# Kernel tuning notes

Hardware: AMD Instinct MI355X
Metric: run time of the kernel (lower is better)

Reference implementation:

```python
import jax, jax.numpy as jnp
from jax import lax
import numpy as np

DATA_DIM, DATA_NUM, CTX_DIM, PB_DIM, HID_DIM, T = 6, 30, 180, 2, 240, 8192


def setup_inputs() -> dict:
    key = jax.random.key(0)
    ks = jax.random.split(key, 12)
    f = lambda k, s: jax.random.normal(k, s, dtype=jnp.float32)
    return {
        "data": f(ks[0], (DATA_NUM, DATA_DIM, T)),
        "W1d": f(ks[1], (HID_DIM, DATA_DIM)) * 0.1,
        "b1d": f(ks[2], (HID_DIM,)) * 0.1,
        "W1p": f(ks[3], (HID_DIM, PB_DIM)) * 0.1,
        "b1p": f(ks[4], (HID_DIM,)) * 0.1,
        "W1c": f(ks[5], (HID_DIM, CTX_DIM)) * 0.05,
        "b1c": f(ks[6], (HID_DIM,)) * 0.1,
        "W2d": f(ks[7], (DATA_DIM, HID_DIM)) * 0.1,
        "b2d": f(ks[8], (DATA_DIM,)) * 0.1,
        "W2c": f(ks[9], (CTX_DIM, HID_DIM)) * 0.05,
        "b2c": f(ks[10], (CTX_DIM,)) * 0.1,
        "pb": f(ks[11], (DATA_NUM, PB_DIM)) * 0.1,
    }


def reference(data, W1d, b1d, W1p, b1p, W1c, b1c, W2d, b2d, W2c, b2c, pb):
    # Teacher-forcing path (GENERATE=False): each timestep's input is data[:, :, t];
    # only ctx is carried through the recurrence.
    # Precompute the time-varying + pb input projections for all steps: [T, B, H]
    pre = (jnp.einsum('bdt,hd->tbh', data, W1d) + b1d
           + (pb @ W1p.T + b1p)[None, :, :])

    def step(ctx, pre_t):
        h = jax.nn.relu(pre_t + ctx @ W1c.T + b1c)   # [B, H]
        out = h @ W2d.T + b2d                        # [B, data_dim]
        new_ctx = h @ W2c.T + b2c                    # [B, ctx_dim]
        return new_ctx, out

    ctx0 = jnp.zeros((data.shape[0], CTX_DIM), dtype=data.dtype)
    _, outs = lax.scan(step, ctx0, pre)              # outs: [T, B, data_dim]
    return jnp.transpose(outs, (1, 0, 2))            # [B, T, data_dim] (stack dim=1)
```

## Files before the change

### kernel.cpp

```cpp
#include <hip/hip_runtime.h>
#include <hip/hip_bf16.h>
#include <stdint.h>


#define T_STEPS 8192
#define HID     240
#define CTX     180
#define KTOT    256
#define HXBUF   4096
#define A_HALVES (256*256)
#define SCRATCH_BYTES (A_HALVES*2 + 16)

typedef __hip_bfloat16 bf16;
typedef _Float16 f16;
typedef _Float16 half8  __attribute__((ext_vector_type(8)));
typedef _Float16 half4v __attribute__((ext_vector_type(4)));
typedef float    f32x4  __attribute__((ext_vector_type(4)));
typedef float    f32x2  __attribute__((ext_vector_type(2)));

#define MFMA16(A,B,C) __builtin_amdgcn_mfma_f32_16x16x32_f16((A),(B),(C),0,0,0)

__device__ __forceinline__ float ldin(const void* p, long i, bool f32) {
    return f32 ? ((const float*)p)[i] : __bfloat162float(((const bf16*)p)[i]);
}
__device__ __forceinline__ unsigned pkbf(float a, float b) {
    unsigned ua = (unsigned)__builtin_bit_cast(unsigned short, __float2bfloat16(a));
    unsigned ub = (unsigned)__builtin_bit_cast(unsigned short, __float2bfloat16(b));
    return ua | (ub << 16);
}
__device__ __forceinline__ void barrier_lds() {
    asm volatile("s_waitcnt lgkmcnt(0)\n\ts_barrier" ::: "memory");
}

__global__ __launch_bounds__(64) void detect_dtype(const void* data, int* flag) {
    unsigned int w  = ((const unsigned int*)data)[threadIdx.x];
    unsigned int lo = w & 0xFFFFu;
    unsigned int ex = (lo >> 7) & 0xFFu;
    unsigned long long huge = __ballot(ex >= 0x8Eu);
    unsigned long long zero = __ballot(lo == 0u);
    if (threadIdx.x == 0) *flag = (huge != 0ull || zero == ~0ull) ? 1 : 0;
}

__global__ __launch_bounds__(256) void build_A(
    const void* __restrict__ W1d, const void* __restrict__ b1d,
    const void* __restrict__ W1p, const void* __restrict__ b1p,
    const void* __restrict__ W1c, const void* __restrict__ b1c,
    const void* __restrict__ W2d, const void* __restrict__ b2d,
    const void* __restrict__ W2c, const void* __restrict__ b2c,
    f16* __restrict__ Aa, const int* __restrict__ flagp)
{
    const bool f32 = (*flagp != 0);
    int idx = blockIdx.x*256 + threadIdx.x;
    int r = idx >> 8, k = idx & 255;
    float v = 0.f;
    if (r < HID) {
        if (k < HID) {
            float acc = 0.f;
            for (int c = 0; c < CTX; ++c)
                acc = fmaf(ldin(W1c, r*CTX+c, f32), ldin(W2c, c*HID+k, f32), acc);
            v = acc;
        } else if (k < 246) {
            v = ldin(W1d, r*6 + (k-240), f32);
        } else if (k == 246) {
            float m0 = 0.f;
            for (int c = 0; c < CTX; ++c)
                m0 = fmaf(ldin(W1c, r*CTX+c, f32), ldin(b2c, c, f32), m0);
            v = ldin(b1d, r, f32) + ldin(b1c, r, f32) + ldin(b1p, r, f32) + m0;
        } else if (k <= 248) {
            v = ldin(W1p, r*2 + (k-247), f32);
        }
    } else if (r < 246) {
        int o = r - 240;
        if (k < HID)       v = ldin(W2d, o*HID + k, f32);
        else if (k == 246) v = ldin(b2d, o, f32);
    }
    Aa[idx] = (f16)v;
}

__device__ __forceinline__ int hx_off(int j, int n) {
    return (j >> 5)*512 + ((((j & 31) >> 3))*16 + n)*8 + (j & 7);
}

__global__ __launch_bounds__(512, 2) void rnn_mfma(
    const void* __restrict__ data,
    const void* __restrict__ b1d, const void* __restrict__ W1p,
    const void* __restrict__ b1p, const void* __restrict__ b1c,
    const void* __restrict__ W1d, const void* __restrict__ pb,
    const f16* __restrict__ Aa, const int* __restrict__ flagp,
    void* __restrict__ out)
{
    const bool f32 = (*flagp != 0);
    const int tid  = threadIdx.x;
    const int w    = tid >> 6;
    const int l    = tid & 63;
    const int n16  = l & 15;
    const int quad = l >> 4;
    const int base = blockIdx.x * 16;
    const int bn   = base + n16;
    const bool bvalid = (bn < 30);

    __shared__ __align__(16) f16 Hx[2*HXBUF];

    {
        int* hz = (int*)Hx;
        for (int i = tid; i < HXBUF; i += 512) hz[i] = 0;
    }
    __syncthreads();

    if (tid < 32) {
        int bsel = tid >> 4, n = tid & 15;
        int nb = base + n; if (nb > 29) nb = 29;
        f16* buf = Hx + bsel*HXBUF;
        buf[3584 + (32+n)*8 + 6] = (f16)1.0f;
        buf[3584 + (32+n)*8 + 7] = (f16)ldin(pb, nb*2+0, f32);
        buf[3584 + (48+n)*8 + 0] = (f16)ldin(pb, nb*2+1, f32);
    }

    for (int p = tid; p < HID*16; p += 512) {
        int n = p / HID, j = p - n*HID;
        int nb = base + n; if (nb > 29) nb = 29;
        float s = ldin(b1d, j, f32) + ldin(b1c, j, f32) + ldin(b1p, j, f32)
                + ldin(W1p, j*2+0, f32)*ldin(pb, nb*2+0, f32)
                + ldin(W1p, j*2+1, f32)*ldin(pb, nb*2+1, f32);
        for (int d = 0; d < 6; ++d)
            s = fmaf(ldin(W1d, j*6+d, f32), ldin(data, ((long)nb*6+d)*T_STEPS, f32), s);
        Hx[hx_off(j, n)] = (f16)fmaxf(s, 0.f);
    }

    const int pn = tid & 15, pd = tid >> 4;
    int pnb = base + pn; if (pnb > 29) pnb = 29;
    const long prow = ((long)pnb*6 + (pd < 6 ? pd : 0))*T_STEPS;
    const int  doff = 3584 + (32+pn)*8 + pd;

    if (tid < 96)
        Hx[doff] = (f16)ldin(data, prow + 1, f32);

    unsigned u0 = 0, u1 = 0;
    if (tid < 96) {
        if (!f32) {
            u0 = ((const unsigned short*)data)[prow + 2];
            u1 = ((const unsigned short*)data)[prow + 3];
        } else {
            u0 = __builtin_bit_cast(unsigned, ((const float*)data)[prow + 2]);
            u1 = __builtin_bit_cast(unsigned, ((const float*)data)[prow + 3]);
        }
    }

    const f16* Ab0 = Aa + (size_t)((w*2+0)*16 + n16)*KTOT + quad*8;
    const f16* Ab1 = Aa + (size_t)((w*2+1)*16 + n16)*KTOT + quad*8;
    half8 a00 = *(const half8*)(Ab0 +   0), a01 = *(const half8*)(Ab0 +  32);
    half8 a02 = *(const half8*)(Ab0 +  64), a03 = *(const half8*)(Ab0 +  96);
    half8 a04 = *(const half8*)(Ab0 + 128), a05 = *(const half8*)(Ab0 + 160);
    half8 a06 = *(const half8*)(Ab0 + 192), a07 = *(const half8*)(Ab0 + 224);
    half8 a10 = *(const half8*)(Ab1 +   0), a11 = *(const half8*)(Ab1 +  32);
    half8 a12 = *(const half8*)(Ab1 +  64), a13 = *(const half8*)(Ab1 +  96);
    half8 a14 = *(const half8*)(Ab1 + 128), a15 = *(const half8*)(Ab1 + 160);
    half8 a16 = *(const half8*)(Ab1 + 192), a17 = *(const half8*)(Ab1 + 224);
    asm volatile("s_waitcnt vmcnt(0)" ::: "memory");
    __syncthreads();

    const f16* hxread0 = Hx + l*8;
    f16* hxw = Hx + w*512 + ((quad>>1)*16 + n16)*8 + 4*(quad&1);

    for (int t2 = 0; t2 < T_STEPS; t2 += 2) {
        #pragma unroll
        for (int s = 0; s < 2; ++s) {
            const int t = t2 + s;
            const int cur = s, nxt = s ^ 1;

            if (tid < 96) {
                unsigned uc = (s == 0) ? u0 : u1;
                float dv = f32 ? __builtin_bit_cast(float, uc)
                               : __builtin_bit_cast(float, uc << 16);
                Hx[nxt*HXBUF + doff] = (f16)dv;
                long g = t + 4; if (g > T_STEPS-1) g = T_STEPS-1;
                unsigned un;
                if (!f32) un = ((const unsigned short*)data)[prow + g];
                else      un = __builtin_bit_cast(unsigned, ((const float*)data)[prow + g]);
                if (s == 0) u0 = un; else u1 = un;
            }

            const f16* hxc = hxread0 + cur*HXBUF;
            half8 b0 = *(const half8*)(hxc +    0);
            half8 b1 = *(const half8*)(hxc +  512);
            half8 b2 = *(const half8*)(hxc + 1024);
            f32x4 c0 = {0.f,0.f,0.f,0.f}, c1 = {0.f,0.f,0.f,0.f};
            half8 b3 = *(const half8*)(hxc + 1536);
            c0 = MFMA16(a00, b0, c0);  c1 = MFMA16(a10, b0, c1);
            half8 b4 = *(const half8*)(hxc + 2048);
            c0 = MFMA16(a01, b1, c0);  c1 = MFMA16(a11, b1, c1);
            half8 b5 = *(const half8*)(hxc + 2560);
            c0 = MFMA16(a02, b2, c0);  c1 = MFMA16(a12, b2, c1);
            half8 b6 = *(const half8*)(hxc + 3072);
            c0 = MFMA16(a03, b3, c0);  c1 = MFMA16(a13, b3, c1);
            half8 b7 = *(const half8*)(hxc + 3584);
            c0 = MFMA16(a04, b4, c0);  c1 = MFMA16(a14, b4, c1);
            c0 = MFMA16(a05, b5, c0);  c1 = MFMA16(a15, b5, c1);
            c0 = MFMA16(a06, b6, c0);  c1 = MFMA16(a16, b6, c1);
            c0 = MFMA16(a07, b7, c0);  c1 = MFMA16(a17, b7, c1);

            f16* hxn = hxw + nxt*HXBUF;
            {
                half4v hv;
                hv.x = (f16)fmaxf(c0.x, 0.f);
                hv.y = (f16)fmaxf(c0.y, 0.f);
                hv.z = (f16)fmaxf(c0.z, 0.f);
                hv.w = (f16)fmaxf(c0.w, 0.f);
                *(half4v*)(hxn) = hv;
            }
            if (w < 7) {
                half4v hv;
                hv.x = (f16)fmaxf(c1.x, 0.f);
                hv.y = (f16)fmaxf(c1.y, 0.f);
                hv.z = (f16)fmaxf(c1.z, 0.f);
                hv.w = (f16)fmaxf(c1.w, 0.f);
                *(half4v*)(hxn + 256) = hv;
            } else if (bvalid) {
                long ob = ((long)bn*T_STEPS + t)*6;
                if (quad == 0) {
                    if (!f32) {
                        bf16* op = (bf16*)out + ob;
                        *(unsigned*)(op)     = pkbf(c1.x, c1.y);
                        *(unsigned*)(op + 2) = pkbf(c1.z, c1.w);
                    } else {
                        float* op = (float*)out + ob;
                        f32x2 p0 = {c1.x, c1.y}; *(f32x2*)(op)     = p0;
                        f32x2 p1 = {c1.z, c1.w}; *(f32x2*)(op + 2) = p1;
                    }
                } else if (quad == 1) {
                    if (!f32) {
                        bf16* op = (bf16*)out + ob;
                        *(unsigned*)(op + 4) = pkbf(c1.x, c1.y);
                    } else {
                        float* op = (float*)out + ob;
                        f32x2 p0 = {c1.x, c1.y}; *(f32x2*)(op + 4) = p0;
                    }
                }
            }
            barrier_lds();
        }
    }
}

extern "C" void kernel_launch(void* const* d_in, const int* in_sizes, int n_in,
                              void* d_out, int out_size, void* d_ws, size_t ws_size,
                              hipStream_t stream) {
    const void* data = d_in[0];
    const void* W1d  = d_in[1];
    const void* b1d  = d_in[2];
    const void* W1p  = d_in[3];
    const void* b1p  = d_in[4];
    const void* W1c  = d_in[5];
    const void* b1c  = d_in[6];
    const void* W2d  = d_in[7];
    const void* b2d  = d_in[8];
    const void* W2c  = d_in[9];
    const void* b2c  = d_in[10];
    const void* pb   = d_in[11];

    size_t need = SCRATCH_BYTES;
    char* scratch;
    if (ws_size >= need) {
        scratch = (char*)d_ws;
    } else {
        size_t out_bytes = (size_t)30*T_STEPS*6*sizeof(bf16);
        scratch = (char*)d_out + ((out_bytes - need) & ~(size_t)255);
    }
    f16* Aa    = (f16*)scratch;
    int* flagp = (int*)(scratch + A_HALVES*2);

    detect_dtype<<<1, 64, 0, stream>>>(data, flagp);
    build_A<<<A_HALVES/256, 256, 0, stream>>>(W1d, b1d, W1p, b1p, W1c, b1c,
                                              W2d, b2d, W2c, b2c, Aa, flagp);
    rnn_mfma<<<2, 512, 0, stream>>>(data, b1d, W1p, b1p, b1c, W1d, pb,
                                    Aa, flagp, d_out);
}
```

Baseline: 3.977 ms.

## Split K dimension across wave pairs with LDS partial-sum exchange

```diff
diff --git a/kernel.cpp b/kernel.cpp
--- a/kernel.cpp
+++ b/kernel.cpp
@@ -8,6 +8,7 @@
 #define CTX     180
 #define KTOT    256
 #define HXBUF   4096
+#define PBUF    4096
 #define A_HALVES (256*256)
 #define SCRATCH_BYTES (A_HALVES*2 + 16)
 
@@ -92,6 +93,9 @@
     const bool f32 = (*flagp != 0);
     const int tid  = threadIdx.x;
     const int w    = tid >> 6;
+    const int P    = w & 3;
+    const int role = w >> 2;
+    const int vw   = P*2 + role;
     const int l    = tid & 63;
     const int n16  = l & 15;
     const int quad = l >> 4;
@@ -99,7 +103,7 @@
     const int bn   = base + n16;
     const bool bvalid = (bn < 30);
 
-    __shared__ __align__(16) f16 Hx[2*HXBUF];
+    __shared__ __align__(16) f16 Hx[2*HXBUF + PBUF];
 
     {
         int* hz = (int*)Hx;
@@ -146,21 +150,22 @@
         }
     }
 
-    const f16* Ab0 = Aa + (size_t)((w*2+0)*16 + n16)*KTOT + quad*8;
-    const f16* Ab1 = Aa + (size_t)((w*2+1)*16 + n16)*KTOT + quad*8;
-    half8 a00 = *(const half8*)(Ab0 +   0), a01 = *(const half8*)(Ab0 +  32);
-    half8 a02 = *(const half8*)(Ab0 +  64), a03 = *(const half8*)(Ab0 +  96);
-    half8 a04 = *(const half8*)(Ab0 + 128), a05 = *(const half8*)(Ab0 + 160);
-    half8 a06 = *(const half8*)(Ab0 + 192), a07 = *(const half8*)(Ab0 + 224);
-    half8 a10 = *(const half8*)(Ab1 +   0), a11 = *(const half8*)(Ab1 +  32);
-    half8 a12 = *(const half8*)(Ab1 +  64), a13 = *(const half8*)(Ab1 +  96);
-    half8 a14 = *(const half8*)(Ab1 + 128), a15 = *(const half8*)(Ab1 + 160);
-    half8 a16 = *(const half8*)(Ab1 + 192), a17 = *(const half8*)(Ab1 + 224);
+    const f16* Ab = Aa + (size_t)((4*P)*16 + n16)*KTOT + role*128 + quad*8;
+    half8 A00 = *(const half8*)(Ab +     0 +  0), A01 = *(const half8*)(Ab +     0 + 32);
+    half8 A02 = *(const half8*)(Ab +     0 + 64), A03 = *(const half8*)(Ab +     0 + 96);
+    half8 A10 = *(const half8*)(Ab +  4096 +  0), A11 = *(const half8*)(Ab +  4096 + 32);
+    half8 A12 = *(const half8*)(Ab +  4096 + 64), A13 = *(const half8*)(Ab +  4096 + 96);
+    half8 A20 = *(const half8*)(Ab +  8192 +  0), A21 = *(const half8*)(Ab +  8192 + 32);
+    half8 A22 = *(const half8*)(Ab +  8192 + 64), A23 = *(const half8*)(Ab +  8192 + 96);
+    half8 A30 = *(const half8*)(Ab + 12288 +  0), A31 = *(const half8*)(Ab + 12288 + 32);
+    half8 A32 = *(const half8*)(Ab + 12288 + 64), A33 = *(const half8*)(Ab + 12288 + 96);
     asm volatile("s_waitcnt vmcnt(0)" ::: "memory");
     __syncthreads();
 
-    const f16* hxread0 = Hx + l*8;
-    f16* hxw = Hx + w*512 + ((quad>>1)*16 + n16)*8 + 4*(quad&1);
+    const f16* hxread0 = Hx + role*2048 + l*8;
+    f16* hxw = Hx + vw*512 + ((quad>>1)*16 + n16)*8 + 4*(quad&1);
+    f16*       pwr = Hx + 2*HXBUF + (P*2 + role)*512     + l*4;
+    const f16* prd = Hx + 2*HXBUF + (P*2 + (role^1))*512 + l*4;
 
     for (int t2 = 0; t2 < T_STEPS; t2 += 2) {
         #pragma unroll
@@ -183,57 +188,74 @@
             const f16* hxc = hxread0 + cur*HXBUF;
             half8 b0 = *(const half8*)(hxc +    0);
             half8 b1 = *(const half8*)(hxc +  512);
+            f32x4 c0 = {0.f,0.f,0.f,0.f}, c1 = {0.f,0.f,0.f,0.f};
+            f32x4 c2 = {0.f,0.f,0.f,0.f}, c3 = {0.f,0.f,0.f,0.f};
             half8 b2 = *(const half8*)(hxc + 1024);
-            f32x4 c0 = {0.f,0.f,0.f,0.f}, c1 = {0.f,0.f,0.f,0.f};
+            c0 = MFMA16(A00, b0, c0);  c1 = MFMA16(A10, b0, c1);
+            c2 = MFMA16(A20, b0, c2);  c3 = MFMA16(A30, b0, c3);
             half8 b3 = *(const half8*)(hxc + 1536);
-            c0 = MFMA16(a00, b0, c0);  c1 = MFMA16(a10, b0, c1);
-            half8 b4 = *(const half8*)(hxc + 2048);
-            c0 = MFMA16(a01, b1, c0);  c1 = MFMA16(a11, b1, c1);
-            half8 b5 = *(const half8*)(hxc + 2560);
-            c0 = MFMA16(a02, b2, c0);  c1 = MFMA16(a12, b2, c1);
-            half8 b6 = *(const half8*)(hxc + 3072);
-            c0 = MFMA16(a03, b3, c0);  c1 = MFMA16(a13, b3, c1);
-            half8 b7 = *(const half8*)(hxc + 3584);
-            c0 = MFMA16(a04, b4, c0);  c1 = MFMA16(a14, b4, c1);
-            c0 = MFMA16(a05, b5, c0);  c1 = MFMA16(a15, b5, c1);
-            c0 = MFMA16(a06, b6, c0);  c1 = MFMA16(a16, b6, c1);
-            c0 = MFMA16(a07, b7, c0);  c1 = MFMA16(a17, b7, c1);
+            c0 = MFMA16(A01, b1, c0);  c1 = MFMA16(A11, b1, c1);
+            c2 = MFMA16(A21, b1, c2);  c3 = MFMA16(A31, b1, c3);
+            c0 = MFMA16(A02, b2, c0);  c1 = MFMA16(A12, b2, c1);
+            c2 = MFMA16(A22, b2, c2);  c3 = MFMA16(A32, b2, c3);
+            c0 = MFMA16(A03, b3, c0);  c1 = MFMA16(A13, b3, c1);
+            c2 = MFMA16(A23, b3, c2);  c3 = MFMA16(A33, b3, c3);
+
+            if (role == 0) {
+                half4v w0; w0.x=(f16)c2.x; w0.y=(f16)c2.y; w0.z=(f16)c2.z; w0.w=(f16)c2.w;
+                half4v w1; w1.x=(f16)c3.x; w1.y=(f16)c3.y; w1.z=(f16)c3.z; w1.w=(f16)c3.w;
+                *(half4v*)(pwr)       = w0;
+                *(half4v*)(pwr + 256) = w1;
+            } else {
+                half4v w0; w0.x=(f16)c0.x; w0.y=(f16)c0.y; w0.z=(f16)c0.z; w0.w=(f16)c0.w;
+                half4v w1; w1.x=(f16)c1.x; w1.y=(f16)c1.y; w1.z=(f16)c1.z; w1.w=(f16)c1.w;
+                *(half4v*)(pwr)       = w0;
+                *(half4v*)(pwr + 256) = w1;
+            }
+            barrier_lds();
+
+            half4v p0 = *(const half4v*)(prd);
+            half4v p1 = *(const half4v*)(prd + 256);
+            f32x4 o0 = (role == 0) ? c0 : c2;
+            f32x4 o1 = (role == 0) ? c1 : c3;
 
             f16* hxn = hxw + nxt*HXBUF;
             {
                 half4v hv;
-                hv.x = (f16)fmaxf(c0.x, 0.f);
-                hv.y = (f16)fmaxf(c0.y, 0.f);
-                hv.z = (f16)fmaxf(c0.z, 0.f);
-                hv.w = (f16)fmaxf(c0.w, 0.f);
+                hv.x = (f16)fmaxf(o0.x + (float)p0.x, 0.f);
+                hv.y = (f16)fmaxf(o0.y + (float)p0.y, 0.f);
+                hv.z = (f16)fmaxf(o0.z + (float)p0.z, 0.f);
+                hv.w = (f16)fmaxf(o0.w + (float)p0.w, 0.f);
                 *(half4v*)(hxn) = hv;
             }
-            if (w < 7) {
+            if (vw < 7) {
                 half4v hv;
-                hv.x = (f16)fmaxf(c1.x, 0.f);
-                hv.y = (f16)fmaxf(c1.y, 0.f);
-                hv.z = (f16)fmaxf(c1.z, 0.f);
-                hv.w = (f16)fmaxf(c1.w, 0.f);
+                hv.x = (f16)fmaxf(o1.x + (float)p1.x, 0.f);
+                hv.y = (f16)fmaxf(o1.y + (float)p1.y, 0.f);
+                hv.z = (f16)fmaxf(o1.z + (float)p1.z, 0.f);
+                hv.w = (f16)fmaxf(o1.w + (float)p1.w, 0.f);
                 *(half4v*)(hxn + 256) = hv;
             } else if (bvalid) {
+                float v0 = o1.x + (float)p1.x, v1 = o1.y + (float)p1.y;
+                float v2 = o1.z + (float)p1.z, v3 = o1.w + (float)p1.w;
                 long ob = ((long)bn*T_STEPS + t)*6;
                 if (quad == 0) {
                     if (!f32) {
                         bf16* op = (bf16*)out + ob;
-                        *(unsigned*)(op)     = pkbf(c1.x, c1.y);
-                        *(unsigned*)(op + 2) = pkbf(c1.z, c1.w);
+                        *(unsigned*)(op)     = pkbf(v0, v1);
+                        *(unsigned*)(op + 2) = pkbf(v2, v3);
                     } else {
                         float* op = (float*)out + ob;
-                        f32x2 p0 = {c1.x, c1.y}; *(f32x2*)(op)     = p0;
-                        f32x2 p1 = {c1.z, c1.w}; *(f32x2*)(op + 2) = p1;
+                        f32x2 q0 = {v0, v1}; *(f32x2*)(op)     = q0;
+                        f32x2 q1 = {v2, v3}; *(f32x2*)(op + 2) = q1;
                     }
                 } else if (quad == 1) {
                     if (!f32) {
                         bf16* op = (bf16*)out + ob;
-                        *(unsigned*)(op + 4) = pkbf(c1.x, c1.y);
+                        *(unsigned*)(op + 4) = pkbf(v0, v1);
                     } else {
                         float* op = (float*)out + ob;
-                        f32x2 p0 = {c1.x, c1.y}; *(f32x2*)(op + 4) = p0;
+                        f32x2 q0 = {v0, v1}; *(f32x2*)(op + 4) = q0;
                     }
                 }
             }
```

Result: slower. 5.643 ms (+41.9%).

## Defer output stores a step, interleave MFMA chains, hoist LDS loads

Applied to the files above, without the earlier changes.

```diff
diff --git a/kernel.cpp b/kernel.cpp
--- a/kernel.cpp
+++ b/kernel.cpp
@@ -30,6 +30,28 @@
 }
 __device__ __forceinline__ void barrier_lds() {
     asm volatile("s_waitcnt lgkmcnt(0)\n\ts_barrier" ::: "memory");
+}
+
+__device__ __forceinline__ void store_out(void* out, bool f32, int quad, long ob, f32x4 v) {
+    if (quad == 0) {
+        if (!f32) {
+            bf16* op = (bf16*)out + ob;
+            *(unsigned*)(op)     = pkbf(v.x, v.y);
+            *(unsigned*)(op + 2) = pkbf(v.z, v.w);
+        } else {
+            float* op = (float*)out + ob;
+            f32x2 p0 = {v.x, v.y}; *(f32x2*)(op)     = p0;
+            f32x2 p1 = {v.z, v.w}; *(f32x2*)(op + 2) = p1;
+        }
+    } else if (quad == 1) {
+        if (!f32) {
+            bf16* op = (bf16*)out + ob;
+            *(unsigned*)(op + 4) = pkbf(v.x, v.y);
+        } else {
+            float* op = (float*)out + ob;
+            f32x2 p0 = {v.x, v.y}; *(f32x2*)(op + 4) = p0;
+        }
+    }
 }
 
 __global__ __launch_bounds__(64) void detect_dtype(const void* data, int* flag) {
@@ -98,6 +120,7 @@
     const int base = blockIdx.x * 16;
     const int bn   = base + n16;
     const bool bvalid = (bn < 30);
+    const long obase = (long)bn * T_STEPS * 6;
 
     __shared__ __align__(16) f16 Hx[2*HXBUF];
 
@@ -136,6 +159,9 @@
         Hx[doff] = (f16)ldin(data, prow + 1, f32);
 
     unsigned u0 = 0, u1 = 0;
+    const unsigned esz = f32 ? 4u : 2u;
+    unsigned voff = (unsigned)((unsigned long)(prow + 4) * esz);
+    const unsigned vmax = (unsigned)((unsigned long)(prow + T_STEPS-1) * esz);
     if (tid < 96) {
         if (!f32) {
             u0 = ((const unsigned short*)data)[prow + 2];
@@ -162,42 +188,56 @@
     const f16* hxread0 = Hx + l*8;
     f16* hxw = Hx + w*512 + ((quad>>1)*16 + n16)*8 + 4*(quad&1);
 
+    f32x4 pend = {0.f, 0.f, 0.f, 0.f};
+
     for (int t2 = 0; t2 < T_STEPS; t2 += 2) {
         #pragma unroll
         for (int s = 0; s < 2; ++s) {
             const int t = t2 + s;
             const int cur = s, nxt = s ^ 1;
 
+            const f16* hxc = hxread0 + cur*HXBUF;
+            half8 b0 = *(const half8*)(hxc +    0);
+            half8 b1 = *(const half8*)(hxc +  512);
+            half8 b2 = *(const half8*)(hxc + 1024);
+            half8 b3 = *(const half8*)(hxc + 1536);
+            half8 b4 = *(const half8*)(hxc + 2048);
+            half8 b5 = *(const half8*)(hxc + 2560);
+            half8 b6 = *(const half8*)(hxc + 3072);
+            half8 b7 = *(const half8*)(hxc + 3584);
+
+            if (w == 7 && bvalid && (s == 1 || t2 > 0))
+                store_out(out, f32, quad, obase + (long)(t-1)*6, pend);
+
             if (tid < 96) {
                 unsigned uc = (s == 0) ? u0 : u1;
                 float dv = f32 ? __builtin_bit_cast(float, uc)
                                : __builtin_bit_cast(float, uc << 16);
                 Hx[nxt*HXBUF + doff] = (f16)dv;
-                long g = t + 4; if (g > T_STEPS-1) g = T_STEPS-1;
                 unsigned un;
-                if (!f32) un = ((const unsigned short*)data)[prow + g];
-                else      un = __builtin_bit_cast(unsigned, ((const float*)data)[prow + g]);
+                if (!f32) un = *(const unsigned short*)((const char*)data + voff);
+                else      un = __builtin_bit_cast(unsigned, *(const float*)((const char*)data + voff));
+                unsigned vn = voff + esz;
+                voff = (vn > vmax) ? vmax : vn;
                 if (s == 0) u0 = un; else u1 = un;
             }
 
-            const f16* hxc = hxread0 + cur*HXBUF;
-            half8 b0 = *(const half8*)(hxc +    0);
-            half8 b1 = *(const half8*)(hxc +  512);
-            half8 b2 = *(const half8*)(hxc + 1024);
             f32x4 c0 = {0.f,0.f,0.f,0.f}, c1 = {0.f,0.f,0.f,0.f};
-            half8 b3 = *(const half8*)(hxc + 1536);
-            c0 = MFMA16(a00, b0, c0);  c1 = MFMA16(a10, b0, c1);
-            half8 b4 = *(const half8*)(hxc + 2048);
-            c0 = MFMA16(a01, b1, c0);  c1 = MFMA16(a11, b1, c1);
-            half8 b5 = *(const half8*)(hxc + 2560);
-            c0 = MFMA16(a02, b2, c0);  c1 = MFMA16(a12, b2, c1);
-            half8 b6 = *(const half8*)(hxc + 3072);
-            c0 = MFMA16(a03, b3, c0);  c1 = MFMA16(a13, b3, c1);
-            half8 b7 = *(const half8*)(hxc + 3584);
-            c0 = MFMA16(a04, b4, c0);  c1 = MFMA16(a14, b4, c1);
-            c0 = MFMA16(a05, b5, c0);  c1 = MFMA16(a15, b5, c1);
-            c0 = MFMA16(a06, b6, c0);  c1 = MFMA16(a16, b6, c1);
-            c0 = MFMA16(a07, b7, c0);  c1 = MFMA16(a17, b7, c1);
+            c0 = MFMA16(a00, b0, c0);
+            c1 = MFMA16(a11, b1, c1);
+            c0 = MFMA16(a01, b1, c0);
+            c1 = MFMA16(a12, b2, c1);
+            c0 = MFMA16(a02, b2, c0);
+            c1 = MFMA16(a13, b3, c1);
+            c0 = MFMA16(a03, b3, c0);
+            c1 = MFMA16(a14, b4, c1);
+            c0 = MFMA16(a04, b4, c0);
+            c1 = MFMA16(a15, b5, c1);
+            c0 = MFMA16(a05, b5, c0);
+            c1 = MFMA16(a16, b6, c1);
+            c0 = MFMA16(a06, b6, c0);
+            c1 = MFMA16(a17, b7, c1);
+            c0 = MFMA16(a07, b7, c0);
 
             f16* hxn = hxw + nxt*HXBUF;
             {
@@ -208,6 +248,8 @@
                 hv.w = (f16)fmaxf(c0.w, 0.f);
                 *(half4v*)(hxn) = hv;
             }
+            c1 = MFMA16(a10, b0, c1);
+
             if (w < 7) {
                 half4v hv;
                 hv.x = (f16)fmaxf(c1.x, 0.f);
@@ -215,31 +257,15 @@
                 hv.z = (f16)fmaxf(c1.z, 0.f);
                 hv.w = (f16)fmaxf(c1.w, 0.f);
                 *(half4v*)(hxn + 256) = hv;
-            } else if (bvalid) {
-                long ob = ((long)bn*T_STEPS + t)*6;
-                if (quad == 0) {
-                    if (!f32) {
-                        bf16* op = (bf16*)out + ob;
-                        *(unsigned*)(op)     = pkbf(c1.x, c1.y);
-                        *(unsigned*)(op + 2) = pkbf(c1.z, c1.w);
-                    } else {
-                        float* op = (float*)out + ob;
-                        f32x2 p0 = {c1.x, c1.y}; *(f32x2*)(op)     = p0;
-                        f32x2 p1 = {c1.z, c1.w}; *(f32x2*)(op + 2) = p1;
-                    }
-                } else if (quad == 1) {
-                    if (!f32) {
-                        bf16* op = (bf16*)out + ob;
-                        *(unsigned*)(op + 4) = pkbf(c1.x, c1.y);
-                    } else {
-                        float* op = (float*)out + ob;
-                        f32x2 p0 = {c1.x, c1.y}; *(f32x2*)(op + 4) = p0;
-                    }
-                }
+            } else {
+                pend = c1;
             }
             barrier_lds();
         }
     }
+
+    if (w == 7 && bvalid)
+        store_out(out, f32, quad, obase + (long)(T_STEPS-1)*6, pend);
 }
 
 extern "C" void kernel_launch(void* const* d_in, const int* in_sizes, int n_in,
```

Result: faster. 3.654 ms, median of 2 (-8.1%).
